# Kernel optimization log

Measured on AMD Instinct MI355X. Metric: run time of the kernel, lower is better.

The kernel has to match this reference:

```python
import jax, jax.numpy as jnp
import numpy as np

B, T, D, H, L = 8, 512, 768, 12, 12
OBS, VOCAB, MAXT, BLK = 128, 6, 4096, 1023
S = 2 * T          # interleaved state/action token sequence
DH = D // H
DFF = 4 * D


def _ln(x, g, b):
    m = jnp.mean(x, -1, keepdims=True)
    v = jnp.mean((x - m) ** 2, -1, keepdims=True)
    return (x - m) * jax.lax.rsqrt(v + 1e-5) * g + b


def setup_inputs() -> dict:
    key = jax.random.key(0)
    ks = jax.random.split(key, 24)
    p = lambda k, shape: (jax.random.normal(k, shape, jnp.float32) * 0.02)
    return {
        'states': jax.random.normal(ks[0], (B, T, OBS), jnp.float32),
        'actions': jax.random.randint(ks[1], (B, T, 1), 0, VOCAB),
        'timesteps': jax.random.randint(ks[2], (B, 1, 1), 0, MAXT + 1),
        'W_s': p(ks[3], (OBS, D)), 'b_s': jnp.zeros((D,), jnp.float32),
        'A_emb': p(ks[4], (VOCAB, D)),
        'pos_emb': p(ks[5], (1, BLK + 1, D)),
        'gpos_emb': p(ks[6], (1, MAXT + 1, D)),
        'ln1_g': jnp.ones((L, D), jnp.float32), 'ln1_b': jnp.zeros((L, D), jnp.float32),
        'Wq': p(ks[7], (L, D, D)), 'bq': jnp.zeros((L, D), jnp.float32),
        'Wk': p(ks[8], (L, D, D)), 'bk': jnp.zeros((L, D), jnp.float32),
        'Wv': p(ks[9], (L, D, D)), 'bv': jnp.zeros((L, D), jnp.float32),
        'Wp': p(ks[10], (L, D, D)), 'bp': jnp.zeros((L, D), jnp.float32),
        'ln2_g': jnp.ones((L, D), jnp.float32), 'ln2_b': jnp.zeros((L, D), jnp.float32),
        'W1': p(ks[11], (L, D, DFF)), 'b1': jnp.zeros((L, DFF), jnp.float32),
        'W2': p(ks[12], (L, DFF, D)), 'b2': jnp.zeros((L, D), jnp.float32),
        'lnf_g': jnp.ones((D,), jnp.float32), 'lnf_b': jnp.zeros((D,), jnp.float32),
    }


def reference(states, actions, timesteps, W_s, b_s, A_emb, pos_emb, gpos_emb,
              ln1_g, ln1_b, Wq, bq, Wk, bk, Wv, bv, Wp, bp,
              ln2_g, ln2_b, W1, b1, W2, b2, lnf_g, lnf_b):
    # encoders
    se = jnp.tanh(states @ W_s + b_s)                       # [B,T,D]
    ae = jnp.tanh(A_emb[actions[..., 0]])                   # [B,T,D]
    # interleave: s0,a0,s1,a1,... -> [B,S,D]
    tok = jnp.stack([se, ae], axis=2).reshape(B, S, D)
    # global positional (one timestep gathered per batch) + local positional
    gpos = gpos_emb[0][timesteps[:, 0, 0]][:, None, :]      # [B,1,D]
    x = tok + gpos + pos_emb[:, :S, :]
    mask = jnp.tril(jnp.ones((S, S), dtype=bool))
    scale = 1.0 / np.sqrt(DH).astype(np.float32)
    for l in range(L):
        h = _ln(x, ln1_g[l], ln1_b[l])
        q = (h @ Wq[l] + bq[l]).reshape(B, S, H, DH)
        k = (h @ Wk[l] + bk[l]).reshape(B, S, H, DH)
        v = (h @ Wv[l] + bv[l]).reshape(B, S, H, DH)
        att = jnp.einsum('bqhd,bkhd->bhqk', q, k) * scale
        att = jnp.where(mask[None, None], att, -jnp.inf)
        att = jax.nn.softmax(att, axis=-1)
        y = jnp.einsum('bhqk,bkhd->bqhd', att, v).reshape(B, S, D)
        x = x + y @ Wp[l] + bp[l]
        h = _ln(x, ln2_g[l], ln2_b[l])
        x = x + jax.nn.gelu(h @ W1[l] + b1[l], approximate=False) @ W2[l] + b2[l]
    x = _ln(x, lnf_g, lnf_b)
    return x[:, ::2, :]                                     # state_output [B,T,D]
```

## Files before the change

### kernel.cpp

```cpp
#include <hip/hip_runtime.h>
#include <hip/hip_bf16.h>

#define B_   8
#define T_   512
#define S_   1024
#define D_   768
#define H_   12
#define DH_  64
#define L_   12
#define DFF_ 3072
#define M_   8192
#define QKVD 2304

typedef float f32x4 __attribute__((ext_vector_type(4)));
typedef short b16x8 __attribute__((ext_vector_type(8)));

#define LDS_CAST(p) ((__attribute__((address_space(3))) void*)(unsigned)(unsigned long long)(p))
#define GBL_CAST(p) ((const __attribute__((address_space(1))) void*)(unsigned long long)(p))

__device__ inline short f2b(float f) {
  unsigned u = __builtin_bit_cast(unsigned, f);
  unsigned r = u + 0x7fffu + ((u >> 16) & 1u);
  return (short)(unsigned short)(r >> 16);
}
__device__ inline float b2f(short s) {
  unsigned u = ((unsigned)(unsigned short)s) << 16;
  return __builtin_bit_cast(float, u);
}
__device__ inline float gelu_f(float v) {
  const float e = __expf(v * (1.5957691216f + 0.0713548162f * v * v));
  return v * e / (e + 1.0f);
}
__device__ inline float tanh_f(float v) {
  const float e = __expf(2.0f * v);
  return 1.0f - 2.0f / (e + 1.0f);
}

__global__ __launch_bounds__(256) void cvt_kernel(const float* __restrict__ in,
                                                  short* __restrict__ out, int n) {
  const int i = (blockIdx.x * 256 + threadIdx.x) * 4;
  if (i < n) {
    const f32x4 v = *(const f32x4*)&in[i];
    out[i] = f2b(v.x); out[i + 1] = f2b(v.y); out[i + 2] = f2b(v.z); out[i + 3] = f2b(v.w);
  }
}

__global__ __launch_bounds__(256) void trconv_kernel(const float* __restrict__ W,
                                                     short* __restrict__ Wt,
                                                     int K, int N) {
  __shared__ float tile[32][33];
  const int k0 = blockIdx.x * 32, n0 = blockIdx.y * 32;
  const int tx = threadIdx.x & 31, ty = threadIdx.x >> 5;
  #pragma unroll
  for (int i = ty; i < 32; i += 8) tile[i][tx] = W[(size_t)(k0 + i) * N + (n0 + tx)];
  __syncthreads();
  #pragma unroll
  for (int i = ty; i < 32; i += 8) Wt[(size_t)(n0 + i) * K + (k0 + tx)] = f2b(tile[tx][i]);
}

__global__ __launch_bounds__(256) void trconv_layer(const float* __restrict__ Wq,
                                                    const float* __restrict__ Wk,
                                                    const float* __restrict__ Wv,
                                                    const float* __restrict__ Wp,
                                                    const float* __restrict__ W1,
                                                    const float* __restrict__ W2,
                                                    short* __restrict__ Dqkv,
                                                    short* __restrict__ Dp,
                                                    short* __restrict__ D1,
                                                    short* __restrict__ D2) {
  __shared__ float tile[32][33];
  int id = blockIdx.x;
  const float* W; short* Dst; int K, N, kt, nt;
  if (id < 2304) {
    const int wsel = id / 576; id -= wsel * 576;
    W   = (wsel == 0) ? Wq : (wsel == 1) ? Wk : (wsel == 2) ? Wv : Wp;
    Dst = (wsel == 3) ? Dp : (Dqkv + (size_t)wsel * D_ * D_);
    K = D_; N = D_; kt = id / 24; nt = id % 24;
  } else if (id < 4608) {
    id -= 2304; W = W1; Dst = D1; K = D_; N = DFF_; kt = id / 96; nt = id % 96;
  } else {
    id -= 4608; W = W2; Dst = D2; K = DFF_; N = D_; kt = id / 24; nt = id % 24;
  }
  const int k0 = kt * 32, n0 = nt * 32;
  const int tx = threadIdx.x & 31, ty = threadIdx.x >> 5;
  #pragma unroll
  for (int i = ty; i < 32; i += 8) tile[i][tx] = W[(size_t)(k0 + i) * N + (n0 + tx)];
  __syncthreads();
  #pragma unroll
  for (int i = ty; i < 32; i += 8) Dst[(size_t)(n0 + i) * K + (k0 + tx)] = f2b(tile[tx][i]);
}

__global__ __launch_bounds__(256) void embed2_kernel(
    const short* __restrict__ se, const int* __restrict__ actions,
    const int* __restrict__ timesteps, const float* __restrict__ A_emb,
    const float* __restrict__ pos_emb, const float* __restrict__ gpos_emb,
    float* __restrict__ x) {
  const int bt = blockIdx.x;
  const int b = bt >> 9, t = bt & 511;
  const int tid = threadIdx.x;
  const int act = actions[bt];
  const int ts = timesteps[b];
  const float* gp = gpos_emb + (size_t)ts * D_;
  #pragma unroll
  for (int i = 0; i < 3; ++i) {
    const int d = tid + i * 256;
    const float sev = b2f(se[(size_t)bt * D_ + d]);
    const float aev = tanhf(A_emb[act * D_ + d]);
    const float g = gp[d];
    const size_t base = ((size_t)b * S_ + 2 * t) * D_ + d;
    x[base]      = sev + g + pos_emb[(2 * t) * D_ + d];
    x[base + D_] = aev + g + pos_emb[(2 * t + 1) * D_ + d];
  }
}

__global__ __launch_bounds__(256) void ln_kernel(const float* __restrict__ x,
                                                 const float* __restrict__ gg,
                                                 const float* __restrict__ bb,
                                                 short* __restrict__ out) {
  __shared__ float red[4];
  const int row = blockIdx.x, tid = threadIdx.x;
  const float* xr = x + (size_t)row * D_;
  float v0 = xr[tid], v1 = xr[tid + 256], v2 = xr[tid + 512];
  float s = v0 + v1 + v2;
  #pragma unroll
  for (int o = 32; o > 0; o >>= 1) s += __shfl_xor(s, o);
  if ((tid & 63) == 0) red[tid >> 6] = s;
  __syncthreads();
  const float mean = (red[0] + red[1] + red[2] + red[3]) * (1.0f / D_);
  __syncthreads();
  const float d0 = v0 - mean, d1 = v1 - mean, d2 = v2 - mean;
  float s2 = d0 * d0 + d1 * d1 + d2 * d2;
  #pragma unroll
  for (int o = 32; o > 0; o >>= 1) s2 += __shfl_xor(s2, o);
  if ((tid & 63) == 0) red[tid >> 6] = s2;
  __syncthreads();
  const float inv = rsqrtf((red[0] + red[1] + red[2] + red[3]) * (1.0f / D_) + 1e-5f);
  short* orow = out + (size_t)row * D_;
  orow[tid]       = f2b(d0 * inv * gg[tid] + bb[tid]);
  orow[tid + 256] = f2b(d1 * inv * gg[tid + 256] + bb[tid + 256]);
  orow[tid + 512] = f2b(d2 * inv * gg[tid + 512] + bb[tid + 512]);
}

template <int MODE>
__global__ __launch_bounds__(256) void reduce2_kernel(
    const float* __restrict__ P, const float* __restrict__ bias,
    float* __restrict__ x, const float* __restrict__ gg,
    const float* __restrict__ bb, short* __restrict__ h,
    float* __restrict__ out) {
  __shared__ float red[4];
  const int row = blockIdx.x, tid = threadIdx.x;
  if (MODE == 2 && (row & 1)) return;
  const float* p0 = P + (size_t)row * D_;
  const float* p1 = P + (size_t)M_ * D_ + (size_t)row * D_;
  float* xr = x + (size_t)row * D_;
  float v0 = xr[tid]       + p0[tid]       + p1[tid]       + bias[tid];
  float v1 = xr[tid + 256] + p0[tid + 256] + p1[tid + 256] + bias[tid + 256];
  float v2 = xr[tid + 512] + p0[tid + 512] + p1[tid + 512] + bias[tid + 512];
  if (MODE == 1) { xr[tid] = v0; xr[tid + 256] = v1; xr[tid + 512] = v2; }
  float s = v0 + v1 + v2;
  #pragma unroll
  for (int o = 32; o > 0; o >>= 1) s += __shfl_xor(s, o);
  if ((tid & 63) == 0) red[tid >> 6] = s;
  __syncthreads();
  const float mean = (red[0] + red[1] + red[2] + red[3]) * (1.0f / D_);
  __syncthreads();
  const float d0 = v0 - mean, d1 = v1 - mean, d2 = v2 - mean;
  float s2 = d0 * d0 + d1 * d1 + d2 * d2;
  #pragma unroll
  for (int o = 32; o > 0; o >>= 1) s2 += __shfl_xor(s2, o);
  if ((tid & 63) == 0) red[tid >> 6] = s2;
  __syncthreads();
  const float inv = rsqrtf((red[0] + red[1] + red[2] + red[3]) * (1.0f / D_) + 1e-5f);
  if (MODE == 1) {
    short* orow = h + (size_t)row * D_;
    orow[tid]       = f2b(d0 * inv * gg[tid] + bb[tid]);
    orow[tid + 256] = f2b(d1 * inv * gg[tid + 256] + bb[tid + 256]);
    orow[tid + 512] = f2b(d2 * inv * gg[tid + 512] + bb[tid + 512]);
  } else {
    const int b = row >> 10, t = (row & 1023) >> 1;
    float* orow = out + ((size_t)b * T_ + t) * D_;
    orow[tid]       = d0 * inv * gg[tid] + bb[tid];
    orow[tid + 256] = d1 * inv * gg[tid + 256] + bb[tid + 256];
    orow[tid + 512] = d2 * inv * gg[tid + 512] + bb[tid + 512];
  }
}

__device__ __forceinline__ void mainloop128(const short* __restrict__ gA,
                                            const short* __restrict__ gB,
                                            int K, int kIters,
                                            short* As, short* Bs,
                                            int wave, int l15, int lq, int wr, int wc,
                                            f32x4 (&acc)[4][4]) {
  auto STAGE = [&](int kt, int buf) {
    const short* a = gA + kt * 32;
    const short* b = gB + kt * 32;
    short* la = As + buf * 4096 + wave * 512;
    short* lb = Bs + buf * 4096 + wave * 512;
    __builtin_amdgcn_global_load_lds(GBL_CAST(a),                  LDS_CAST(la),        16, 0, 0);
    __builtin_amdgcn_global_load_lds(GBL_CAST(a + (size_t)64 * K), LDS_CAST(la + 2048), 16, 0, 0);
    __builtin_amdgcn_global_load_lds(GBL_CAST(b),                  LDS_CAST(lb),        16, 0, 0);
    __builtin_amdgcn_global_load_lds(GBL_CAST(b + (size_t)64 * K), LDS_CAST(lb + 2048), 16, 0, 0);
  };
  STAGE(0, 0);
  if (kIters > 1) STAGE(1, 1);
  const int coff = (lq ^ ((l15 >> 1) & 3)) * 8;
  int b0 = 0, b1 = 1, b2 = 2;
  for (int kt = 0; kt < kIters; ++kt) {
    if (kt + 1 < kIters) {
      asm volatile("s_waitcnt vmcnt(4)" ::: "memory");
    } else {
      asm volatile("s_waitcnt vmcnt(0)" ::: "memory");
    }
    __builtin_amdgcn_s_barrier();
    __builtin_amdgcn_sched_barrier(0);
    if (kt + 2 < kIters) STAGE(kt + 2, b2);
    const short* Ab = As + b0 * 4096;
    const short* Bb = Bs + b0 * 4096;
    b16x8 af[4], bfr[4];
    #pragma unroll
    for (int i = 0; i < 4; ++i)
      af[i] = *(const b16x8*)&Ab[(wr * 64 + i * 16 + l15) * 32 + coff];
    #pragma unroll
    for (int j = 0; j < 4; ++j)
      bfr[j] = *(const b16x8*)&Bb[(wc * 64 + j * 16 + l15) * 32 + coff];
    __builtin_amdgcn_s_setprio(1);
    #pragma unroll
    for (int i = 0; i < 4; ++i)
      #pragma unroll
      for (int j = 0; j < 4; ++j)
        acc[i][j] = __builtin_amdgcn_mfma_f32_16x16x32_bf16(af[i], bfr[j], acc[i][j], 0, 0, 0);
    __builtin_amdgcn_s_setprio(0);
    const int t = b0; b0 = b1; b1 = b2; b2 = t;
  }
}

template <int EPI>
__global__ __launch_bounds__(256) void gemm_bf16(const short* __restrict__ A,
                                                 const short* __restrict__ Bt,
                                                 const float* __restrict__ bias,
                                                 short* __restrict__ Cb,
                                                 int M, int N, int K) {
  __shared__ __align__(16) short As[12288];
  __shared__ __align__(16) short Bs[12288];
  const int tid = threadIdx.x;
  const int wave = tid >> 6, lane = tid & 63;
  const int l15 = lane & 15, lq = lane >> 4;
  const int wr = wave >> 1, wc = wave & 1;
  const int row0 = blockIdx.x * 128, col0 = blockIdx.y * 128;
  const int acs = ((tid & 3) ^ ((tid >> 3) & 3)) * 8;

  const short* gA = A + (size_t)(row0 + (tid >> 2)) * K + acs;
  const short* gB = Bt + (size_t)(col0 + (tid >> 2)) * K + acs;
  f32x4 acc[4][4] = {};
  mainloop128(gA, gB, K, K / 32, As, Bs, wave, l15, lq, wr, wc, acc);

  #pragma unroll
  for (int i = 0; i < 4; ++i) {
    #pragma unroll
    for (int j = 0; j < 4; ++j) {
      const int col = col0 + wc * 64 + j * 16 + l15;
      const float bv = bias[col];
      #pragma unroll
      for (int r = 0; r < 4; ++r) {
        const int row = row0 + wr * 64 + i * 16 + lq * 4 + r;
        const float v = acc[i][j][r] + bv;
        const size_t idx = (size_t)row * N + col;
        if (EPI == 1) Cb[idx] = f2b(gelu_f(v));
        else          Cb[idx] = f2b(tanh_f(v));
      }
    }
  }
}

__global__ __launch_bounds__(256) void gemm_splitk(const short* __restrict__ A,
                                                   const short* __restrict__ Bt,
                                                   float* __restrict__ P,
                                                   int M, int N, int K, int KC) {
  __shared__ __align__(16) short As[12288];
  __shared__ __align__(16) short Bs[12288];
  const int tid = threadIdx.x;
  const int wave = tid >> 6, lane = tid & 63;
  const int l15 = lane & 15, lq = lane >> 4;
  const int wr = wave >> 1, wc = wave & 1;
  const int row0 = blockIdx.x * 128, col0 = blockIdx.y * 128;
  const int k0 = blockIdx.z * KC;
  const int acs = ((tid & 3) ^ ((tid >> 3) & 3)) * 8;

  const short* gA = A + (size_t)(row0 + (tid >> 2)) * K + acs + k0;
  const short* gB = Bt + (size_t)(col0 + (tid >> 2)) * K + acs + k0;
  f32x4 acc[4][4] = {};
  mainloop128(gA, gB, K, KC / 32, As, Bs, wave, l15, lq, wr, wc, acc);

  float* Pz = P + (size_t)blockIdx.z * M * N;
  #pragma unroll
  for (int i = 0; i < 4; ++i) {
    #pragma unroll
    for (int j = 0; j < 4; ++j) {
      const int col = col0 + wc * 64 + j * 16 + l15;
      #pragma unroll
      for (int r = 0; r < 4; ++r) {
        const int row = row0 + wr * 64 + i * 16 + lq * 4 + r;
        Pz[(size_t)row * N + col] = acc[i][j][r];
      }
    }
  }
}

__global__ __launch_bounds__(256) void gemm_qkv(const short* __restrict__ A,
                                                const short* __restrict__ Bt,
                                                const float* __restrict__ bq,
                                                const float* __restrict__ bk,
                                                const float* __restrict__ bv,
                                                short* __restrict__ Cb, int K) {
  __shared__ __align__(16) short As[12288];
  __shared__ __align__(16) short Bs[12288];
  const int tid = threadIdx.x;
  const int wave = tid >> 6, lane = tid & 63;
  const int l15 = lane & 15, lq = lane >> 4;
  const int wr = wave >> 1, wc = wave & 1;
  const int row0 = blockIdx.x * 128, col0 = blockIdx.y * 128;
  const int seg = col0 / D_;
  const float* bias = (seg == 0) ? bq : (seg == 1) ? bk : bv;
  const float scale = (seg == 0) ? 0.125f : 1.0f;
  const int acs = ((tid & 3) ^ ((tid >> 3) & 3)) * 8;

  const short* gA = A + (size_t)(row0 + (tid >> 2)) * K + acs;
  const short* gB = Bt + (size_t)(col0 + (tid >> 2)) * K + acs;
  f32x4 acc[4][4] = {};
  mainloop128(gA, gB, K, K / 32, As, Bs, wave, l15, lq, wr, wc, acc);

  #pragma unroll
  for (int i = 0; i < 4; ++i) {
    #pragma unroll
    for (int j = 0; j < 4; ++j) {
      const int col = col0 + wc * 64 + j * 16 + l15;
      const float bv = bias[col - seg * D_];
      #pragma unroll
      for (int r = 0; r < 4; ++r) {
        const int row = row0 + wr * 64 + i * 16 + lq * 4 + r;
        Cb[(size_t)row * QKVD + col] = f2b((acc[i][j][r] + bv) * scale);
      }
    }
  }
}

__global__ __launch_bounds__(256) void gemm64(const short* __restrict__ A,
                                              const short* __restrict__ Bt,
                                              const float* __restrict__ bias,
                                              float* __restrict__ Xres,
                                              int M, int N, int K) {
  __shared__ __align__(16) short As[6144];
  __shared__ __align__(16) short Bs[12288];
  const int tid = threadIdx.x;
  const int wave = tid >> 6, lane = tid & 63;
  const int l15 = lane & 15, lq = lane >> 4;
  const int wr = wave >> 1, wc = wave & 1;
  const int row0 = blockIdx.x * 64, col0 = blockIdx.y * 128;
  const int acs = ((tid & 3) ^ ((tid >> 3) & 3)) * 8;

  const short* gA = A + (size_t)(row0 + (tid >> 2)) * K + acs;
  const short* gB = Bt + (size_t)(col0 + (tid >> 2)) * K + acs;

  auto STAGE = [&](int kt, int buf) {
    const short* a = gA + kt * 32;
    const short* b = gB + kt * 32;
    short* la = As + buf * 2048 + wave * 512;
    short* lb = Bs + buf * 4096 + wave * 512;
    __builtin_amdgcn_global_load_lds(GBL_CAST(a),                  LDS_CAST(la),        16, 0, 0);
    __builtin_amdgcn_global_load_lds(GBL_CAST(b),                  LDS_CAST(lb),        16, 0, 0);
    __builtin_amdgcn_global_load_lds(GBL_CAST(b + (size_t)64 * K), LDS_CAST(lb + 2048), 16, 0, 0);
  };

  f32x4 acc[2][4] = {};
  const int kIters = K / 32;
  STAGE(0, 0);
  if (kIters > 1) STAGE(1, 1);
  const int coff = (lq ^ ((l15 >> 1) & 3)) * 8;
  int b0 = 0, b1 = 1, b2 = 2;
  for (int kt = 0; kt < kIters; ++kt) {
    if (kt + 1 < kIters) {
      asm volatile("s_waitcnt vmcnt(3)" ::: "memory");
    } else {
      asm volatile("s_waitcnt vmcnt(0)" ::: "memory");
    }
    __builtin_amdgcn_s_barrier();
    __builtin_amdgcn_sched_barrier(0);
    if (kt + 2 < kIters) STAGE(kt + 2, b2);
    const short* Ab = As + b0 * 2048;
    const short* Bb = Bs + b0 * 4096;
    b16x8 af[2], bfr[4];
    #pragma unroll
    for (int i = 0; i < 2; ++i)
      af[i] = *(const b16x8*)&Ab[(wr * 32 + i * 16 + l15) * 32 + coff];
    #pragma unroll
    for (int j = 0; j < 4; ++j)
      bfr[j] = *(const b16x8*)&Bb[(wc * 64 + j * 16 + l15) * 32 + coff];
    __builtin_amdgcn_s_setprio(1);
    #pragma unroll
    for (int i = 0; i < 2; ++i)
      #pragma unroll
      for (int j = 0; j < 4; ++j)
        acc[i][j] = __builtin_amdgcn_mfma_f32_16x16x32_bf16(af[i], bfr[j], acc[i][j], 0, 0, 0);
    __builtin_amdgcn_s_setprio(0);
    const int t = b0; b0 = b1; b1 = b2; b2 = t;
  }
  #pragma unroll
  for (int i = 0; i < 2; ++i) {
    #pragma unroll
    for (int j = 0; j < 4; ++j) {
      const int col = col0 + wc * 64 + j * 16 + l15;
      const float bv = bias[col];
      #pragma unroll
      for (int r = 0; r < 4; ++r) {
        const int row = row0 + wr * 32 + i * 16 + lq * 4 + r;
        Xres[(size_t)row * N + col] += acc[i][j][r] + bv;
      }
    }
  }
}

__global__ __launch_bounds__(256) void attn_kernel(const short* __restrict__ qkv,
                                                   short* __restrict__ yb) {
  __shared__ __align__(16) short Ks[2][4096];
  __shared__ __align__(16) short Vt[2][64 * 72];
  __shared__ __align__(16) short Ps[4][16 * 88];

  const int bh = blockIdx.x, pair = blockIdx.y;
  const int h = bh % H_, b = bh / H_;
  const int tid = threadIdx.x, wave = tid >> 6, lane = tid & 63;
  const int l15 = lane & 15, lq = lane >> 4;

  const int r0 = tid >> 3, c0 = tid & 7;
  const int r1 = (tid + 256) >> 3;
  const int vkey = tid >> 2, vdhg = tid & 3;

  for (int t2 = 0; t2 < 2; ++t2) {
    const int qt = t2 ? (15 - pair) : pair;
    const int nkt = qt + 1;
    const int qrow0 = qt * 64 + wave * 16;

    const short* qp = qkv + (size_t)(b * S_ + qrow0 + l15) * QKVD + h * 64 + lq * 8;
    const b16x8 qf0 = *(const b16x8*)qp;
    const b16x8 qf1 = *(const b16x8*)(qp + 32);

    f32x4 o[4] = {};
    float lacc[4] = {0.f, 0.f, 0.f, 0.f};

    auto stage = [&](int kt, int s) {
      const int kbase = kt * 64;
      const short* gk0 = qkv + (size_t)(b * S_ + kbase + r0) * QKVD + D_ + h * 64 + ((c0 ^ (r0 & 7)) * 8);
      __builtin_amdgcn_global_load_lds(GBL_CAST(gk0), LDS_CAST(&Ks[s][wave * 512]), 16, 0, 0);
      const short* gk1 = qkv + (size_t)(b * S_ + kbase + r1) * QKVD + D_ + h * 64 + ((c0 ^ (r1 & 7)) * 8);
      __builtin_amdgcn_global_load_lds(GBL_CAST(gk1), LDS_CAST(&Ks[s][2048 + wave * 512]), 16, 0, 0);
      const short* gv = qkv + (size_t)(b * S_ + kbase + vkey) * QKVD + 2 * D_ + h * 64 + vdhg * 16;
      const b16x8 v0 = *(const b16x8*)gv;
      const b16x8 v1 = *(const b16x8*)(gv + 8);
      #pragma unroll
      for (int e = 0; e < 8; ++e) Vt[s][(vdhg * 16 + e) * 72 + vkey] = v0[e];
      #pragma unroll
      for (int e = 0; e < 8; ++e) Vt[s][(vdhg * 16 + 8 + e) * 72 + vkey] = v1[e];
    };

    stage(0, 0);
    __syncthreads();

    for (int kt = 0; kt < nkt; ++kt) {
      const int cur = kt & 1;
      if (kt + 1 < nkt) stage(kt + 1, cur ^ 1);
      const int kbase = kt * 64;
      const bool needmask = (kt == qt);

      f32x4 s4[4];
      #pragma unroll
      for (int j = 0; j < 4; ++j) {
        const int krow = j * 16 + l15;
        const b16x8 kf0 = *(const b16x8*)&Ks[cur][krow * 64 + ((lq ^ (krow & 7)) * 8)];
        const b16x8 kf1 = *(const b16x8*)&Ks[cur][krow * 64 + (((4 + lq) ^ (krow & 7)) * 8)];
        f32x4 z = {};
        z = __builtin_amdgcn_mfma_f32_16x16x32_bf16(qf0, kf0, z, 0, 0, 0);
        s4[j] = __builtin_amdgcn_mfma_f32_16x16x32_bf16(qf1, kf1, z, 0, 0, 0);
      }

      #pragma unroll
      for (int r = 0; r < 4; ++r) {
        const int q = qrow0 + lq * 4 + r;
        float psum = 0.f;
        #pragma unroll
        for (int j = 0; j < 4; ++j) {
          float pp = __expf(s4[j][r]);
          if (needmask && (kbase + j * 16 + l15 > q)) pp = 0.f;
          psum += pp;
          Ps[wave][(lq * 4 + r) * 88 + j * 16 + l15] = f2b(pp);
        }
        lacc[r] += psum;
      }

      #pragma unroll
      for (int c = 0; c < 2; ++c) {
        const b16x8 pf = *(const b16x8*)&Ps[wave][l15 * 88 + c * 32 + lq * 8];
        #pragma unroll
        for (int jn = 0; jn < 4; ++jn) {
          const b16x8 vf = *(const b16x8*)&Vt[cur][(jn * 16 + l15) * 72 + c * 32 + lq * 8];
          o[jn] = __builtin_amdgcn_mfma_f32_16x16x32_bf16(pf, vf, o[jn], 0, 0, 0);
        }
      }
      __syncthreads();
    }

    #pragma unroll
    for (int r = 0; r < 4; ++r) {
      #pragma unroll
      for (int ofs = 1; ofs < 16; ofs <<= 1) lacc[r] += __shfl_xor(lacc[r], ofs);
      lacc[r] = 1.0f / lacc[r];
    }

    #pragma unroll
    for (int jn = 0; jn < 4; ++jn) {
      #pragma unroll
      for (int r = 0; r < 4; ++r) {
        const int q = qrow0 + lq * 4 + r;
        const int dh = jn * 16 + l15;
        yb[(size_t)(b * S_ + q) * D_ + h * 64 + dh] = f2b(o[jn][r] * lacc[r]);
      }
    }
  }
}

extern "C" void kernel_launch(void* const* d_in, const int* in_sizes, int n_in,
                              void* d_out, int out_size, void* d_ws, size_t ws_size,
                              hipStream_t stream) {
  (void)in_sizes; (void)n_in; (void)out_size; (void)ws_size;
  const float* states    = (const float*)d_in[0];
  const int*   actions   = (const int*)d_in[1];
  const int*   timesteps = (const int*)d_in[2];
  const float* W_s       = (const float*)d_in[3];
  const float* b_s       = (const float*)d_in[4];
  const float* A_emb     = (const float*)d_in[5];
  const float* pos_emb   = (const float*)d_in[6];
  const float* gpos_emb  = (const float*)d_in[7];
  const float* ln1_g     = (const float*)d_in[8];
  const float* ln1_b     = (const float*)d_in[9];
  const float* Wq        = (const float*)d_in[10];
  const float* bq        = (const float*)d_in[11];
  const float* Wk        = (const float*)d_in[12];
  const float* bk        = (const float*)d_in[13];
  const float* Wv        = (const float*)d_in[14];
  const float* bv        = (const float*)d_in[15];
  const float* Wp        = (const float*)d_in[16];
  const float* bp        = (const float*)d_in[17];
  const float* ln2_g     = (const float*)d_in[18];
  const float* ln2_b     = (const float*)d_in[19];
  const float* W1        = (const float*)d_in[20];
  const float* b1        = (const float*)d_in[21];
  const float* W2        = (const float*)d_in[22];
  const float* b2        = (const float*)d_in[23];
  const float* lnf_g     = (const float*)d_in[24];
  const float* lnf_b     = (const float*)d_in[25];
  float* out = (float*)d_out;

  char* p = (char*)d_ws;
  float* x    = (float*)p; p += (size_t)M_ * D_ * 4;
  short* h    = (short*)p; p += (size_t)M_ * D_ * 2;
  short* qkv  = (short*)p; p += (size_t)M_ * QKVD * 2;
  short* y    = (short*)p; p += (size_t)M_ * D_ * 2;
  short* gbf  = (short*)p; p += (size_t)M_ * DFF_ * 2;
  short* wqkvt= (short*)p; p += (size_t)QKVD * D_ * 2;
  short* wpt  = (short*)p; p += (size_t)D_ * D_ * 2;
  short* w1t  = (short*)p; p += (size_t)D_ * DFF_ * 2;
  short* w2t  = (short*)p; p += (size_t)D_ * DFF_ * 2;
  float* Pbuf = (float*)qkv;
  short* sbf  = qkv;
  short* wst  = qkv + (size_t)4096 * 128;
  short* se   = gbf;

  cvt_kernel<<<(B_ * T_ * 128) / 1024, 256, 0, stream>>>(states, sbf, B_ * T_ * 128);
  trconv_kernel<<<dim3(4, 24), 256, 0, stream>>>(W_s, wst, 128, D_);
  gemm_bf16<4><<<dim3(32, 6), 256, 0, stream>>>(sbf, wst, b_s, se, 4096, D_, 128);
  embed2_kernel<<<B_ * T_, 256, 0, stream>>>(se, actions, timesteps, A_emb, pos_emb, gpos_emb, x);
  ln_kernel<<<M_, 256, 0, stream>>>(x, ln1_g, ln1_b, h);

  for (int l = 0; l < L_; ++l) {
    trconv_layer<<<6912, 256, 0, stream>>>(
        Wq + (size_t)l * D_ * D_, Wk + (size_t)l * D_ * D_,
        Wv + (size_t)l * D_ * D_, Wp + (size_t)l * D_ * D_,
        W1 + (size_t)l * D_ * DFF_, W2 + (size_t)l * D_ * DFF_,
        wqkvt, wpt, w1t, w2t);

    gemm_qkv<<<dim3(M_ / 128, QKVD / 128), 256, 0, stream>>>(h, wqkvt, bq + l * D_, bk + l * D_, bv + l * D_, qkv, D_);
    attn_kernel<<<dim3(B_ * H_, 8), 256, 0, stream>>>(qkv, y);
    gemm64<<<dim3(M_ / 64, D_ / 128), 256, 0, stream>>>(y, wpt, bp + l * D_, x, M_, D_, D_);
    ln_kernel<<<M_, 256, 0, stream>>>(x, ln2_g + l * D_, ln2_b + l * D_, h);
    gemm_bf16<1><<<dim3(M_ / 128, DFF_ / 128), 256, 0, stream>>>(h, w1t, b1 + l * DFF_, gbf, M_, DFF_, D_);
    gemm_splitk<<<dim3(M_ / 128, D_ / 128, 2), 256, 0, stream>>>(gbf, w2t, Pbuf, M_, D_, DFF_, DFF_ / 2);
    if (l < L_ - 1) {
      reduce2_kernel<1><<<M_, 256, 0, stream>>>(Pbuf, b2 + l * D_, x,
                                                ln1_g + (l + 1) * D_, ln1_b + (l + 1) * D_, h, nullptr);
    } else {
      reduce2_kernel<2><<<M_, 256, 0, stream>>>(Pbuf, b2 + l * D_, x, lnf_g, lnf_b, nullptr, out);
    }
  }
}
```

Before: 3.040 ms.

## Replace QKV, FFN1 and FFN2 GEMMs with a 256x256-tile 512-thread kernel

Adds a templated gemm256 kernel with 256x256 output tiles, 8 waves, BK=64 double-buffered direct-to-LDS loads with an XOR swizzle, and s_setprio around the MFMA bursts. It replaces the 128x128 QKV, FFN-up (GELU) and split-K FFN-down kernels, with the epilogue picked by a template parameter. Larger tiles raise arithmetic intensity and cut global/LDS traffic per FLOP. In exchange, grids shrink (e.g. 32x9 for QKV, 32x3x2 for FFN2), which can underfill the 256 CUs, and register pressure rises with 128 accumulators per thread.

```diff
diff --git a/kernel.cpp b/kernel.cpp
--- a/kernel.cpp
+++ b/kernel.cpp
@@ -182,6 +182,137 @@
     orow[tid]       = d0 * inv * gg[tid] + bb[tid];
     orow[tid + 256] = d1 * inv * gg[tid + 256] + bb[tid + 256];
     orow[tid + 512] = d2 * inv * gg[tid + 512] + bb[tid + 512];
+  }
+}
+
+template <int EPI>
+__global__ __launch_bounds__(512, 2) void gemm256(const short* __restrict__ A,
+                                                  const short* __restrict__ Bt,
+                                                  const float* __restrict__ bias0,
+                                                  const float* __restrict__ bias1,
+                                                  const float* __restrict__ bias2,
+                                                  short* __restrict__ Cb,
+                                                  float* __restrict__ Pf,
+                                                  int M, int N, int K, int KC) {
+  __shared__ __align__(16) short As[2][16384];
+  __shared__ __align__(16) short Bs[2][16384];
+  const int tid = threadIdx.x;
+  const int wave = tid >> 6, lane = tid & 63;
+  const int l15 = lane & 15, lq = lane >> 4;
+  const int wr = wave >> 2, wc = wave & 3;
+  const int row0 = blockIdx.x * 256, col0 = blockIdx.y * 256;
+  const int k0 = blockIdx.z * KC;
+  const int nk = KC / 64;
+
+  const int srow = tid >> 3;
+  const int sch = ((tid & 7) ^ (srow & 7)) * 8;
+  const short* gA = A + (size_t)(row0 + srow) * K + k0 + sch;
+  const short* gB = Bt + (size_t)(col0 + srow) * K + k0 + sch;
+
+  auto STAGE = [&](int kt, int buf) {
+    #pragma unroll
+    for (int j = 0; j < 4; ++j) {
+      __builtin_amdgcn_global_load_lds(GBL_CAST(gA + (size_t)(j * 64) * K + kt * 64),
+                                       LDS_CAST(&As[buf][j * 4096 + wave * 512]), 16, 0, 0);
+      __builtin_amdgcn_global_load_lds(GBL_CAST(gB + (size_t)(j * 64) * K + kt * 64),
+                                       LDS_CAST(&Bs[buf][j * 4096 + wave * 512]), 16, 0, 0);
+    }
+  };
+
+  f32x4 acc[8][4] = {};
+  STAGE(0, 0);
+  if (nk > 1) STAGE(1, 1);
+
+  const int axr = wr * 128 + l15;
+  const int bxr = wc * 64 + l15;
+  const int swz = l15 & 7;
+
+  for (int t = 0; t < nk; ++t) {
+    const int buf = t & 1;
+    if (t + 1 < nk) { asm volatile("s_waitcnt vmcnt(8)" ::: "memory"); }
+    else            { asm volatile("s_waitcnt vmcnt(0)" ::: "memory"); }
+    __builtin_amdgcn_s_barrier();
+    __builtin_amdgcn_sched_barrier(0);
+
+    b16x8 af[8], bf[4];
+    #pragma unroll
+    for (int m = 0; m < 8; ++m)
+      af[m] = *(const b16x8*)&As[buf][(axr + m * 16) * 64 + (lq ^ swz) * 8];
+    #pragma unroll
+    for (int n = 0; n < 4; ++n)
+      bf[n] = *(const b16x8*)&Bs[buf][(bxr + n * 16) * 64 + (lq ^ swz) * 8];
+    asm volatile("s_waitcnt lgkmcnt(0)" ::: "memory");
+    __builtin_amdgcn_sched_barrier(0);
+    __builtin_amdgcn_s_setprio(1);
+    #pragma unroll
+    for (int m = 0; m < 8; ++m)
+      #pragma unroll
+      for (int n = 0; n < 4; ++n)
+        acc[m][n] = __builtin_amdgcn_mfma_f32_16x16x32_bf16(af[m], bf[n], acc[m][n], 0, 0, 0);
+    __builtin_amdgcn_s_setprio(0);
+
+    #pragma unroll
+    for (int m = 0; m < 8; ++m)
+      af[m] = *(const b16x8*)&As[buf][(axr + m * 16) * 64 + ((4 + lq) ^ swz) * 8];
+    #pragma unroll
+    for (int n = 0; n < 4; ++n)
+      bf[n] = *(const b16x8*)&Bs[buf][(bxr + n * 16) * 64 + ((4 + lq) ^ swz) * 8];
+    asm volatile("s_waitcnt lgkmcnt(0)" ::: "memory");
+    __builtin_amdgcn_sched_barrier(0);
+    __builtin_amdgcn_s_barrier();
+    __builtin_amdgcn_sched_barrier(0);
+    if (t + 2 < nk) STAGE(t + 2, buf);
+    __builtin_amdgcn_s_setprio(1);
+    #pragma unroll
+    for (int m = 0; m < 8; ++m)
+      #pragma unroll
+      for (int n = 0; n < 4; ++n)
+        acc[m][n] = __builtin_amdgcn_mfma_f32_16x16x32_bf16(af[m], bf[n], acc[m][n], 0, 0, 0);
+    __builtin_amdgcn_s_setprio(0);
+  }
+
+  if (EPI == 0) {
+    const int seg = col0 / D_;
+    const float* bias = (seg == 0) ? bias0 : (seg == 1) ? bias1 : bias2;
+    const float scale = (seg == 0) ? 0.125f : 1.0f;
+    #pragma unroll
+    for (int m = 0; m < 8; ++m)
+      #pragma unroll
+      for (int n = 0; n < 4; ++n) {
+        const int col = col0 + wc * 64 + n * 16 + l15;
+        const float bv = bias[col - seg * D_];
+        #pragma unroll
+        for (int r = 0; r < 4; ++r) {
+          const int row = row0 + wr * 128 + m * 16 + lq * 4 + r;
+          Cb[(size_t)row * QKVD + col] = f2b((acc[m][n][r] + bv) * scale);
+        }
+      }
+  } else if (EPI == 1) {
+    #pragma unroll
+    for (int m = 0; m < 8; ++m)
+      #pragma unroll
+      for (int n = 0; n < 4; ++n) {
+        const int col = col0 + wc * 64 + n * 16 + l15;
+        const float bv = bias0[col];
+        #pragma unroll
+        for (int r = 0; r < 4; ++r) {
+          const int row = row0 + wr * 128 + m * 16 + lq * 4 + r;
+          Cb[(size_t)row * N + col] = f2b(gelu_f(acc[m][n][r] + bv));
+        }
+      }
+  } else {
+    float* Pz = Pf + (size_t)blockIdx.z * M * N;
+    #pragma unroll
+    for (int m = 0; m < 8; ++m)
+      #pragma unroll
+      for (int n = 0; n < 4; ++n) {
+        const int col = col0 + wc * 64 + n * 16 + l15;
+        #pragma unroll
+        for (int r = 0; r < 4; ++r) {
+          const int row = row0 + wr * 128 + m * 16 + lq * 4 + r;
+          Pz[(size_t)row * N + col] = acc[m][n][r];
+        }
+      }
   }
 }
 
@@ -267,78 +398,6 @@
         const size_t idx = (size_t)row * N + col;
         if (EPI == 1) Cb[idx] = f2b(gelu_f(v));
         else          Cb[idx] = f2b(tanh_f(v));
-      }
-    }
-  }
-}
-
-__global__ __launch_bounds__(256) void gemm_splitk(const short* __restrict__ A,
-                                                   const short* __restrict__ Bt,
-                                                   float* __restrict__ P,
-                                                   int M, int N, int K, int KC) {
-  __shared__ __align__(16) short As[12288];
-  __shared__ __align__(16) short Bs[12288];
-  const int tid = threadIdx.x;
-  const int wave = tid >> 6, lane = tid & 63;
-  const int l15 = lane & 15, lq = lane >> 4;
-  const int wr = wave >> 1, wc = wave & 1;
-  const int row0 = blockIdx.x * 128, col0 = blockIdx.y * 128;
-  const int k0 = blockIdx.z * KC;
-  const int acs = ((tid & 3) ^ ((tid >> 3) & 3)) * 8;
-
-  const short* gA = A + (size_t)(row0 + (tid >> 2)) * K + acs + k0;
-  const short* gB = Bt + (size_t)(col0 + (tid >> 2)) * K + acs + k0;
-  f32x4 acc[4][4] = {};
-  mainloop128(gA, gB, K, KC / 32, As, Bs, wave, l15, lq, wr, wc, acc);
-
-  float* Pz = P + (size_t)blockIdx.z * M * N;
-  #pragma unroll
-  for (int i = 0; i < 4; ++i) {
-    #pragma unroll
-    for (int j = 0; j < 4; ++j) {
-      const int col = col0 + wc * 64 + j * 16 + l15;
-      #pragma unroll
-      for (int r = 0; r < 4; ++r) {
-        const int row = row0 + wr * 64 + i * 16 + lq * 4 + r;
-        Pz[(size_t)row * N + col] = acc[i][j][r];
-      }
-    }
-  }
-}
-
-__global__ __launch_bounds__(256) void gemm_qkv(const short* __restrict__ A,
-                                                const short* __restrict__ Bt,
-                                                const float* __restrict__ bq,
-                                                const float* __restrict__ bk,
-                                                const float* __restrict__ bv,
-                                                short* __restrict__ Cb, int K) {
-  __shared__ __align__(16) short As[12288];
-  __shared__ __align__(16) short Bs[12288];
-  const int tid = threadIdx.x;
-  const int wave = tid >> 6, lane = tid & 63;
-  const int l15 = lane & 15, lq = lane >> 4;
-  const int wr = wave >> 1, wc = wave & 1;
-  const int row0 = blockIdx.x * 128, col0 = blockIdx.y * 128;
-  const int seg = col0 / D_;
-  const float* bias = (seg == 0) ? bq : (seg == 1) ? bk : bv;
-  const float scale = (seg == 0) ? 0.125f : 1.0f;
-  const int acs = ((tid & 3) ^ ((tid >> 3) & 3)) * 8;
-
-  const short* gA = A + (size_t)(row0 + (tid >> 2)) * K + acs;
-  const short* gB = Bt + (size_t)(col0 + (tid >> 2)) * K + acs;
-  f32x4 acc[4][4] = {};
-  mainloop128(gA, gB, K, K / 32, As, Bs, wave, l15, lq, wr, wc, acc);
-
-  #pragma unroll
-  for (int i = 0; i < 4; ++i) {
-    #pragma unroll
-    for (int j = 0; j < 4; ++j) {
-      const int col = col0 + wc * 64 + j * 16 + l15;
-      const float bv = bias[col - seg * D_];
-      #pragma unroll
-      for (int r = 0; r < 4; ++r) {
-        const int row = row0 + wr * 64 + i * 16 + lq * 4 + r;
-        Cb[(size_t)row * QKVD + col] = f2b((acc[i][j][r] + bv) * scale);
       }
     }
   }
@@ -586,12 +645,15 @@
         W1 + (size_t)l * D_ * DFF_, W2 + (size_t)l * D_ * DFF_,
         wqkvt, wpt, w1t, w2t);
 
-    gemm_qkv<<<dim3(M_ / 128, QKVD / 128), 256, 0, stream>>>(h, wqkvt, bq + l * D_, bk + l * D_, bv + l * D_, qkv, D_);
+    gemm256<0><<<dim3(M_ / 256, QKVD / 256), 512, 0, stream>>>(
+        h, wqkvt, bq + l * D_, bk + l * D_, bv + l * D_, qkv, nullptr, M_, QKVD, D_, D_);
     attn_kernel<<<dim3(B_ * H_, 8), 256, 0, stream>>>(qkv, y);
     gemm64<<<dim3(M_ / 64, D_ / 128), 256, 0, stream>>>(y, wpt, bp + l * D_, x, M_, D_, D_);
     ln_kernel<<<M_, 256, 0, stream>>>(x, ln2_g + l * D_, ln2_b + l * D_, h);
-    gemm_bf16<1><<<dim3(M_ / 128, DFF_ / 128), 256, 0, stream>>>(h, w1t, b1 + l * DFF_, gbf, M_, DFF_, D_);
-    gemm_splitk<<<dim3(M_ / 128, D_ / 128, 2), 256, 0, stream>>>(gbf, w2t, Pbuf, M_, D_, DFF_, DFF_ / 2);
+    gemm256<1><<<dim3(M_ / 256, DFF_ / 256), 512, 0, stream>>>(
+        h, w1t, b1 + l * DFF_, nullptr, nullptr, gbf, nullptr, M_, DFF_, D_, D_);
+    gemm256<2><<<dim3(M_ / 256, D_ / 256, 2), 512, 0, stream>>>(
+        gbf, w2t, nullptr, nullptr, nullptr, nullptr, Pbuf, M_, D_, DFF_, DFF_ / 2);
     if (l < L_ - 1) {
       reduce2_kernel<1><<<M_, 256, 0, stream>>>(Pbuf, b2 + l * D_, x,
                                                 ln1_g + (l + 1) * D_, ln1_b + (l + 1) * D_, h, nullptr);
```

New measurement: 3.178 ms. +4.6%, slower.
